# Kernel tuning notes

Hardware: AMD Instinct MI355X
Metric: run time of the kernel (lower is better)

The kernel has to match this reference:

```python
import jax, jax.numpy as jnp
import numpy as np

B, V, C, H, W, D, G = 1, 5, 32, 128, 160, 48, 1


def _bilinear_sample(fea, x, y):
    # fea: [B,C,H,W]; x,y: [B,N] pixel coords (grid_sample align_corners=True, zero padding)
    Bb, Cc, Hh, Ww = fea.shape
    x0 = jnp.floor(x); y0 = jnp.floor(y)
    x1 = x0 + 1.0; y1 = y0 + 1.0
    wx1 = x - x0; wx0 = 1.0 - wx1
    wy1 = y - y0; wy0 = 1.0 - wy1
    flat = fea.reshape(Bb, Cc, Hh * Ww)
    def gather(xi, yi):
        valid = (xi >= 0) & (xi <= Ww - 1) & (yi >= 0) & (yi <= Hh - 1)
        xc = jnp.clip(xi, 0, Ww - 1).astype(jnp.int32)
        yc = jnp.clip(yi, 0, Hh - 1).astype(jnp.int32)
        idx = (yc * Ww + xc)[:, None, :]                      # [B,1,N]
        g = jnp.take_along_axis(flat, idx, axis=2)            # [B,C,N]
        return g * valid[:, None, :].astype(fea.dtype)
    return (gather(x0, y0) * (wx0 * wy0)[:, None, :]
          + gather(x1, y0) * (wx1 * wy0)[:, None, :]
          + gather(x0, y1) * (wx0 * wy1)[:, None, :]
          + gather(x1, y1) * (wx1 * wy1)[:, None, :])          # [B,C,N]


def _homo_warp(src_fea, src_proj, ref_proj, depth_values):
    # src_fea [B,C,H,W]; src_proj/ref_proj [B,4,4]; depth_values [B,D,H,W]
    Bb, Cc, Hh, Ww = src_fea.shape
    Dd = depth_values.shape[1]
    proj = src_proj @ jnp.linalg.inv(ref_proj)
    rot, trans = proj[:, :3, :3], proj[:, :3, 3:4]
    yy, xx = jnp.meshgrid(jnp.arange(Hh, dtype=src_fea.dtype),
                          jnp.arange(Ww, dtype=src_fea.dtype), indexing='ij')
    xyz = jnp.stack([xx.ravel(), yy.ravel(), jnp.ones(Hh * Ww, src_fea.dtype)], 0)  # [3,HW]
    rot_xyz = jnp.einsum('bij,jn->bin', rot, xyz)                                    # [B,3,HW]
    d = depth_values.reshape(Bb, 1, Dd, Hh * Ww)
    pxyz = rot_xyz[:, :, None, :] * d + trans[:, :, :, None]                         # [B,3,D,HW]
    px = (pxyz[:, 0] / pxyz[:, 2]).reshape(Bb, -1)
    py = (pxyz[:, 1] / pxyz[:, 2]).reshape(Bb, -1)
    warped = _bilinear_sample(src_fea, px, py)                                       # [B,C,D*HW]
    return warped.reshape(Bb, Cc, Dd, Hh, Ww)


def _pixelwise_net(sim, w0, b0, w1, b1, w2, b2):
    # sim [B,G,D,H,W]; 1x1x1 convs; BatchNorm at default init in eval is identity
    x = jax.nn.relu(jnp.einsum('oc,bcdhw->bodhw', w0, sim) + b0[None, :, None, None, None])
    x = jax.nn.relu(jnp.einsum('oc,bcdhw->bodhw', w1, x) + b1[None, :, None, None, None])
    x = jnp.einsum('oc,bcdhw->bodhw', w2, x) + b2[None, :, None, None, None]
    p = jax.nn.sigmoid(x[:, 0])                       # [B,D,H,W]
    return jnp.max(p, axis=1, keepdims=True)          # [B,1,H,W]


def _fuse_proj(p):
    # p [B,2,4,4] -> extrinsics with K folded into top 3x4
    top = jnp.einsum('bij,bjk->bik', p[:, 1, :3, :3], p[:, 0, :3, :4])
    return p[:, 0].at[:, :3, :4].set(top)


def _forward(features, proj_matrices, depth_values, w0, b0, w1, b1, w2, b2, reg_w, reg_b, num_depth):
    ref_fea = features[0]
    Bb, Cc, Hh, Ww = ref_fea.shape
    ref_proj = _fuse_proj(proj_matrices[:, 0])
    ref_vol = ref_fea.reshape(Bb, G, Cc // G, 1, Hh, Ww)
    sim_sum = 0.0
    wsum = 1e-5
    vw_list = []
    for i in range(1, features.shape[0]):
        src_proj = _fuse_proj(proj_matrices[:, i])
        warped = _homo_warp(features[i], src_proj, ref_proj, depth_values)
        warped = warped.reshape(Bb, G, Cc // G, num_depth, Hh, Ww)
        sim = (warped * ref_vol).mean(2)              # [B,G,D,H,W]
        vw = _pixelwise_net(sim, w0, b0, w1, b1, w2, b2)   # [B,1,H,W]
        vw_list.append(vw)
        sim_sum = sim_sum + sim * vw[:, None]
        wsum = wsum + vw[:, None]
    sim = sim_sum / wsum
    cost = jax.lax.conv_general_dilated(sim, reg_w, (1, 1, 1), 'SAME',
                                        dimension_numbers=('NCDHW', 'OIDHW', 'NCDHW'))
    prob_volume_pre = cost[:, 0] + reg_b[0]           # [B,D,H,W]
    prob = jax.nn.softmax(prob_volume_pre, axis=1)
    idx = jnp.argmax(prob, axis=1, keepdims=True)
    depth = jnp.take_along_axis(depth_values, idx, axis=1)[:, 0]   # winner-take-all depth
    conf = jnp.max(prob, axis=1)
    view_weights = jnp.concatenate(vw_list, axis=1)
    return depth, conf, prob, view_weights


def setup_inputs() -> dict:
    key = jax.random.key(0)
    ks = jax.random.split(key, 6)
    features = jax.random.normal(ks[0], (V, B, C, H, W), jnp.float32)
    # Plausible camera geometry: identity-ish extrinsics + pinhole intrinsics
    K = np.eye(4, dtype=np.float32)
    K[0, 0] = K[1, 1] = 150.0; K[0, 2] = W / 2.0; K[1, 2] = H / 2.0
    mats = []
    for v in range(V):
        E = np.eye(4, dtype=np.float32)
        a = 0.01 * v
        ca, sa = np.cos(a), np.sin(a)
        E[:3, :3] = np.array([[ca, 0, sa], [0, 1, 0], [-sa, 0, ca]], np.float32)
        E[0, 3] = -5.0 * v
        mats.append(np.stack([E, K], 0))
    proj_matrices = jnp.asarray(np.stack(mats, 0)[None])  # [1,V,2,4,4]
    depth_values = jnp.broadcast_to(
        jnp.linspace(425.0, 935.0, D, dtype=jnp.float32).reshape(1, D, 1, 1), (B, D, H, W)) * jnp.ones((B, D, H, W), jnp.float32)
    return {
        'features': features,
        'proj_matrices': proj_matrices,
        'depth_values': depth_values,
        'w0': jax.random.normal(ks[1], (16, G), jnp.float32) * 0.1,
        'b0': jnp.zeros((16,), jnp.float32),
        'w1': jax.random.normal(ks[2], (8, 16), jnp.float32) * 0.1,
        'b1': jnp.zeros((8,), jnp.float32),
        'w2': jax.random.normal(ks[3], (1, 8), jnp.float32) * 0.1,
        'b2': jnp.zeros((1,), jnp.float32),
        'reg_w': jax.random.normal(ks[4], (1, G, 3, 3, 3), jnp.float32) * 0.1,
        'reg_b': jnp.zeros((1,), jnp.float32),
        'num_depth': D,
    }


def reference(features, proj_matrices, depth_values, w0, b0, w1, b1, w2, b2, reg_w, reg_b, num_depth):
    return _forward(features, proj_matrices, depth_values, w0, b0, w1, b1, w2, b2, reg_w, reg_b, num_depth)
```

## Files before the change

kernel.cpp:

```cpp
#include <hip/hip_runtime.h>
#include <hip/hip_bf16.h>
#include <math.h>

#define W_  160
#define H_  128
#define HW  20480
#define D_  48
#define C_  32
#define NV  4

#define TX  16
#define TY  4
#define TXH 18
#define TYH 6
#define NCOL (TXH*TYH)
#define GD  4
#define GDS 12

template<int CTRL>
__device__ __forceinline__ float dpp_add(float s) {
  int t = __builtin_amdgcn_update_dpp(0, __float_as_int(s), CTRL, 0xF, 0xF, true);
  return s + __int_as_float(t);
}

__device__ __forceinline__ unsigned ordf(float f) {
  unsigned b = __float_as_uint(f);
  return b ^ (((int)b >> 31) | 0x80000000u);
}
__device__ __forceinline__ float deordf(unsigned u) {
  unsigned b = (u & 0x80000000u) ? (u ^ 0x80000000u) : ~u;
  return __uint_as_float(b);
}

__device__ __forceinline__ void fuse_proj(const float* pm, float* P) {
  const float* E = pm;
  const float* K = pm + 16;
  for (int r = 0; r < 3; ++r)
    for (int c = 0; c < 4; ++c)
      P[r*4+c] = K[r*4+0]*E[0*4+c] + K[r*4+1]*E[1*4+c] + K[r*4+2]*E[2*4+c];
  for (int c = 0; c < 4; ++c) P[12+c] = E[12+c];
}

__device__ void invert4(const float* m, float* invOut) {
  float inv[16];
  inv[0]  =  m[5]*m[10]*m[15] - m[5]*m[11]*m[14] - m[9]*m[6]*m[15] + m[9]*m[7]*m[14] + m[13]*m[6]*m[11] - m[13]*m[7]*m[10];
  inv[4]  = -m[4]*m[10]*m[15] + m[4]*m[11]*m[14] + m[8]*m[6]*m[15] - m[8]*m[7]*m[14] - m[12]*m[6]*m[11] + m[12]*m[7]*m[10];
  inv[8]  =  m[4]*m[9]*m[15]  - m[4]*m[11]*m[13] - m[8]*m[5]*m[15] + m[8]*m[7]*m[13] + m[12]*m[5]*m[11] - m[12]*m[7]*m[9];
  inv[12] = -m[4]*m[9]*m[14]  + m[4]*m[10]*m[13] + m[8]*m[5]*m[14] - m[8]*m[6]*m[13] - m[12]*m[5]*m[10] + m[12]*m[6]*m[9];
  inv[1]  = -m[1]*m[10]*m[15] + m[1]*m[11]*m[14] + m[9]*m[2]*m[15] - m[9]*m[3]*m[14] - m[13]*m[2]*m[11] + m[13]*m[3]*m[10];
  inv[5]  =  m[0]*m[10]*m[15] - m[0]*m[11]*m[14] - m[8]*m[2]*m[15] + m[8]*m[3]*m[14] + m[12]*m[2]*m[11] - m[12]*m[3]*m[10];
  inv[9]  = -m[0]*m[9]*m[15]  + m[0]*m[11]*m[13] + m[8]*m[1]*m[15] - m[8]*m[3]*m[13] - m[12]*m[1]*m[11] + m[12]*m[3]*m[9];
  inv[13] =  m[0]*m[9]*m[14]  - m[0]*m[10]*m[13] - m[8]*m[1]*m[14] + m[8]*m[2]*m[13] + m[12]*m[1]*m[10] - m[12]*m[2]*m[9];
  inv[2]  =  m[1]*m[6]*m[15]  - m[1]*m[7]*m[14]  - m[5]*m[2]*m[15] + m[5]*m[3]*m[14] + m[13]*m[2]*m[7]  - m[13]*m[3]*m[6];
  inv[6]  = -m[0]*m[6]*m[15]  + m[0]*m[7]*m[14]  + m[4]*m[2]*m[15] - m[4]*m[3]*m[14] - m[12]*m[2]*m[7]  + m[12]*m[3]*m[6];
  inv[10] =  m[0]*m[5]*m[15]  - m[0]*m[7]*m[13]  - m[4]*m[1]*m[15] + m[4]*m[3]*m[13] + m[12]*m[1]*m[7]  - m[12]*m[3]*m[5];
  inv[14] = -m[0]*m[5]*m[14]  + m[0]*m[6]*m[13]  + m[4]*m[1]*m[14] - m[4]*m[2]*m[13] - m[12]*m[1]*m[6]  + m[12]*m[2]*m[5];
  inv[3]  = -m[1]*m[6]*m[11]  + m[1]*m[7]*m[10]  + m[5]*m[2]*m[11] - m[5]*m[3]*m[10] - m[9]*m[2]*m[7]   + m[9]*m[3]*m[6];
  inv[7]  =  m[0]*m[6]*m[11]  - m[0]*m[7]*m[10]  - m[4]*m[2]*m[11] + m[4]*m[3]*m[10] + m[8]*m[2]*m[7]   - m[8]*m[3]*m[6];
  inv[11] = -m[0]*m[5]*m[11]  + m[0]*m[7]*m[9]   + m[4]*m[1]*m[11] - m[4]*m[3]*m[9]  - m[8]*m[1]*m[7]   + m[8]*m[3]*m[5];
  inv[15] =  m[0]*m[5]*m[10]  - m[0]*m[6]*m[9]   - m[4]*m[1]*m[10] + m[4]*m[2]*m[9]  + m[8]*m[1]*m[6]   - m[8]*m[2]*m[5];
  float det = m[0]*inv[0] + m[1]*inv[4] + m[2]*inv[8] + m[3]*inv[12];
  det = 1.0f / det;
  for (int i = 0; i < 16; i++) invOut[i] = inv[i] * det;
}

__global__ void __launch_bounds__(256)
k_prep(const float* __restrict__ feat, const float* __restrict__ pm,
       float* __restrict__ tf, float* __restrict__ xf,
       unsigned* __restrict__ vwu) {
  __shared__ float tile[C_][64+1];
  int v  = blockIdx.y;
  int p0 = blockIdx.x * 64;
  int t  = threadIdx.x;

  if (v == 0) vwu[blockIdx.x*256 + t] = 0u;

  int pl = t & 63;
  int cg = t >> 6;
  const float* src = feat + (size_t)v*C_*HW + p0 + pl;
  #pragma unroll
  for (int k = 0; k < 8; ++k) {
    int c = cg*8 + k;
    tile[c][pl] = src[(size_t)c*HW];
  }
  __syncthreads();

  int pp = t >> 2;
  int co = (t & 3) * 8;
  float4 a, b;
  a.x = tile[co+0][pp]; a.y = tile[co+1][pp]; a.z = tile[co+2][pp]; a.w = tile[co+3][pp];
  b.x = tile[co+4][pp]; b.y = tile[co+5][pp]; b.z = tile[co+6][pp]; b.w = tile[co+7][pp];
  float* dst = tf + ((size_t)v*HW + p0 + pp)*C_ + co;
  *(float4*)dst = a;
  *(float4*)(dst+4) = b;

  if (blockIdx.x == 0 && v == 0) {
    if (t < 64) tf[(size_t)5*HW*C_ + t] = 0.0f;
    if (t == 0) {
      float Pr[16], Pinv[16], Ps[16], M[16];
      fuse_proj(pm, Pr);
      invert4(Pr, Pinv);
      for (int vv = 1; vv <= NV; ++vv) {
        fuse_proj(pm + vv*32, Ps);
        for (int r = 0; r < 4; ++r)
          for (int c = 0; c < 4; ++c) {
            float acc = 0.f;
            for (int k = 0; k < 4; ++k) acc += Ps[r*4+k]*Pinv[k*4+c];
            M[r*4+c] = acc;
          }
        float* o = xf + (vv-1)*12;
        o[0]=M[0];  o[1]=M[1];  o[2]=M[2];
        o[3]=M[4];  o[4]=M[5];  o[5]=M[6];
        o[6]=M[8];  o[7]=M[9];  o[8]=M[10];
        o[9]=M[3];  o[10]=M[7]; o[11]=M[11];
      }
    }
  }
}

template<int KX>
__device__ __forceinline__ void build_tab(
    const char* tfb, int chb, int ZB, float4 rfc,
    int xmin, int ymin, int ch, float* tabp) {
  #pragma unroll
  for (int t = 0; t < KX*3; ++t) {
    int xi = xmin + t/3;
    int yi = ymin + t%3;
    bool valid = ((unsigned)xi < (unsigned)W_) && ((unsigned)yi < (unsigned)H_);
    int off = valid ? (yi*W_ + xi)*(C_*4) : ZB;
    float4 a = *(const float4*)(tfb + off + chb);
    float d = a.x*rfc.x + a.y*rfc.y + a.z*rfc.z + a.w*rfc.w;
    d = dpp_add<0xB1>(d);
    d = dpp_add<0x4E>(d);
    d = dpp_add<0x141>(d);
    if (ch == (t & 7)) tabp[t] = d;
  }
}

__global__ void __launch_bounds__(256)
k_warp(const float* __restrict__ tf, const float* __restrict__ dv,
       const float* __restrict__ xf, float* __restrict__ sim4) {
  __shared__ float dtab[4][8][37];

  int lane = threadIdx.x & 63;
  int wv = threadIdx.x >> 6;
  int ch = lane & 7;
  int pix = (lane >> 3) & 7;
  int wvg = __builtin_amdgcn_readfirstlane((blockIdx.x*256 + threadIdx.x) >> 6);
  const int PGPV = HW/8;
  int pg = wvg % PGPV;
  int v  = wvg / PGPV;
  int p  = pg*8 + pix;

  float xpix = (float)(p % W_);
  float ypix = (float)(p / W_);

  const float* M = xf + v*12;
  float rx = M[0]*xpix + M[1]*ypix + M[2];
  float ry = M[3]*xpix + M[4]*ypix + M[5];
  float rz = M[6]*xpix + M[7]*ypix + M[8];
  float t0 = M[9], t1 = M[10], t2 = M[11];

  float4 rfc = *(const float4*)(tf + (size_t)p*C_ + ch*4);
  rfc.x *= (1.0f/(float)C_); rfc.y *= (1.0f/(float)C_);
  rfc.z *= (1.0f/(float)C_); rfc.w *= (1.0f/(float)C_);

  const char* tfb = (const char*)(tf + (size_t)(v+1)*HW*C_);
  const int chb = ch*16;
  const int ZB = (4-v)*HW*C_*4;

  float depE0 = dv[p];
  float depE1 = dv[(size_t)47*HW + p];
  float dpk[6];
  #pragma unroll
  for (int k = 0; k < 6; ++k) dpk[k] = dv[(size_t)(k*8 + ch)*HW + p];

  float Z0 = rz*depE0 + t2, Z1 = rz*depE1 + t2;
  float iz0 = 1.0f / Z0,     iz1 = 1.0f / Z1;
  float pxa = (rx*depE0 + t0) * iz0, pya = (ry*depE0 + t1) * iz0;
  float pxb = (rx*depE1 + t0) * iz1, pyb = (ry*depE1 + t1) * iz1;
  int xmin = (int)floorf(fminf(pxa, pxb));
  int ymin = (int)floorf(fminf(pya, pyb));
  int Nx = (int)floorf(fmaxf(pxa, pxb)) - xmin + 2;
  int Ny = (int)floorf(fmaxf(pya, pyb)) - ymin + 2;

  float dmn = fminf(depE0, depE1), dmx = fmaxf(depE0, depE1);
  bool ok = (Nx <= 12) && (Ny <= 3) && (Z0*Z1 > 0.0f);
  #pragma unroll
  for (int k = 0; k < 6; ++k) ok = ok && (dpk[k] >= dmn) && (dpk[k] <= dmx);

  float* simv = sim4 + (size_t)p*4 + v;

  if (__all(ok)) {
    float* tabp = dtab[wv][pix];
    int xhi;
    if (__all(Nx <= 5)) {
      build_tab<5>(tfb, chb, ZB, rfc, xmin, ymin, ch, tabp);
      xhi = xmin + 3;
    } else if (__all(Nx <= 8)) {
      build_tab<8>(tfb, chb, ZB, rfc, xmin, ymin, ch, tabp);
      xhi = xmin + 6;
    } else {
      build_tab<12>(tfb, chb, ZB, rfc, xmin, ymin, ch, tabp);
      xhi = xmin + 10;
    }

    #pragma unroll
    for (int k = 0; k < 6; ++k) {
      float dep = dpk[k];
      float Z  = rz*dep + t2;
      float zr = 1.0f / Z;
      float px = (rx*dep + t0) * zr;
      float py = (ry*dep + t1) * zr;
      int xi = (int)floorf(px);
      int yi = (int)floorf(py);
      xi = min(max(xi, xmin), xhi);
      yi = min(max(yi, ymin), ymin + 1);
      float wx1 = px - (float)xi;
      float wy1 = py - (float)yi;
      float wx0 = 1.0f - wx1, wy0 = 1.0f - wy1;
      int idx = (xi - xmin)*3 + (yi - ymin);
      float t00 = tabp[idx];
      float t01 = tabp[idx + 3];
      float t10 = tabp[idx + 1];
      float t11 = tabp[idx + 4];
      float s = wx0*wy0*t00 + wx1*wy0*t01 + wx0*wy1*t10 + wx1*wy1*t11;
      if (ch == ch) ;
      simv[(size_t)(k*8 + ch)*HW*4] = s;
    }
  } else {
    const float* tff  = tf + (size_t)(v+1)*HW*C_;
    const float* refp = tf + (size_t)p*C_;
    const int ZE = (4-v)*HW*C_;
    #pragma unroll 1
    for (int k = 0; k < 6; ++k) {
      float dep = dpk[k];
      float Z  = rz*dep + t2;
      float px = (rx*dep + t0) / Z;
      float py = (ry*dep + t1) / Z;
      float x0f = floorf(px), y0f = floorf(py);
      float wx1 = px - x0f, wy1 = py - y0f;
      float wx0 = 1.0f - wx1, wy0 = 1.0f - wy1;
      int x0 = (int)x0f, y0 = (int)y0f;
      int x1 = x0 + 1,   y1 = y0 + 1;
      bool vx0 = ((unsigned)x0 <= (unsigned)(W_-1));
      bool vx1 = ((unsigned)x1 <= (unsigned)(W_-1));
      bool vy0 = ((unsigned)y0 <= (unsigned)(H_-1));
      bool vy1 = ((unsigned)y1 <= (unsigned)(H_-1));
      int cx0 = min(max(x0, 0), W_-1);
      int cx1 = min(max(x1, 0), W_-1);
      int cy0 = min(max(y0, 0), H_-1);
      int cy1 = min(max(y1, 0), H_-1);
      int o00 = (vx0 && vy0) ? (cy0*W_+cx0)*C_ : ZE;
      int o01 = (vx1 && vy0) ? (cy0*W_+cx1)*C_ : ZE;
      int o10 = (vx0 && vy1) ? (cy1*W_+cx0)*C_ : ZE;
      int o11 = (vx1 && vy1) ? (cy1*W_+cx1)*C_ : ZE;
      float a00=0.f, a01=0.f, a10=0.f, a11=0.f;
      #pragma unroll 1
      for (int q = 0; q < 8; ++q) {
        float4 rq = *(const float4*)(refp + q*4);
        float4 c0 = *(const float4*)(tff + o00 + q*4);
        float4 c1 = *(const float4*)(tff + o01 + q*4);
        float4 c2 = *(const float4*)(tff + o10 + q*4);
        float4 c3 = *(const float4*)(tff + o11 + q*4);
        a00 += c0.x*rq.x + c0.y*rq.y + c0.z*rq.z + c0.w*rq.w;
        a01 += c1.x*rq.x + c1.y*rq.y + c1.z*rq.z + c1.w*rq.w;
        a10 += c2.x*rq.x + c2.y*rq.y + c2.z*rq.z + c2.w*rq.w;
        a11 += c3.x*rq.x + c3.y*rq.y + c3.z*rq.z + c3.w*rq.w;
      }
      float s = (wx0*wy0*a00 + wx1*wy0*a01 + wx0*wy1*a10 + wx1*wy1*a11)
                * (1.0f/(float)C_);
      simv[(size_t)(k*8 + ch)*HW*4] = s;
    }
  }
}

__global__ void __launch_bounds__(256)
k_mlp(const float* __restrict__ sim4,
      const float* __restrict__ w0, const float* __restrict__ b0,
      const float* __restrict__ w1, const float* __restrict__ b1,
      const float* __restrict__ w2, const float* __restrict__ b2,
      unsigned* __restrict__ vwu) {
  int idx = blockIdx.x*blockDim.x + threadIdx.x;
  if (idx >= D_*HW) return;
  int p = idx % HW;

  float4 s4 = *(const float4*)(sim4 + (size_t)idx*4);

  float y0, y1, y2, y3;
  {
    float acc[4][8];
    #pragma unroll
    for (int j = 0; j < 8; ++j) {
      float bb = b1[j];
      acc[0][j] = bb; acc[1][j] = bb; acc[2][j] = bb; acc[3][j] = bb;
    }
    #pragma unroll
    for (int o = 0; o < 16; ++o) {
      float wo = w0[o], bo = b0[o];
      float h0 = fmaxf(fmaf(wo, s4.x, bo), 0.0f);
      float h1 = fmaxf(fmaf(wo, s4.y, bo), 0.0f);
      float h2 = fmaxf(fmaf(wo, s4.z, bo), 0.0f);
      float h3 = fmaxf(fmaf(wo, s4.w, bo), 0.0f);
      #pragma unroll
      for (int j = 0; j < 8; ++j) {
        float w = w1[j*16+o];
        acc[0][j] = fmaf(w, h0, acc[0][j]);
        acc[1][j] = fmaf(w, h1, acc[1][j]);
        acc[2][j] = fmaf(w, h2, acc[2][j]);
        acc[3][j] = fmaf(w, h3, acc[3][j]);
      }
    }
    float b2v = b2[0];
    y0 = b2v; y1 = b2v; y2 = b2v; y3 = b2v;
    #pragma unroll
    for (int j = 0; j < 8; ++j) {
      float w = w2[j];
      y0 = fmaf(w, fmaxf(acc[0][j], 0.0f), y0);
      y1 = fmaf(w, fmaxf(acc[1][j], 0.0f), y1);
      y2 = fmaf(w, fmaxf(acc[2][j], 0.0f), y2);
      y3 = fmaf(w, fmaxf(acc[3][j], 0.0f), y3);
    }
  }
  atomicMax(&vwu[0*HW + p], ordf(y0));
  atomicMax(&vwu[1*HW + p], ordf(y1));
  atomicMax(&vwu[2*HW + p], ordf(y2));
  atomicMax(&vwu[3*HW + p], ordf(y3));
}

__global__ void __launch_bounds__(256)
k_fusecv(const float* __restrict__ sim4, const unsigned* __restrict__ vwu,
         const float* __restrict__ rw, const float* __restrict__ rb,
         float* __restrict__ cost) {
  __shared__ float svw[NV][NCOL];
  __shared__ float sinvw[NCOL];
  __shared__ int   sgpc[NCOL];
  __shared__ float sfus[GDS+2][TYH][TXH+1];

  int tid = threadIdx.x;
  int gx0 = blockIdx.x*TX;
  int gy0 = blockIdx.y*TY;
  int g   = blockIdx.z;

  if (tid < NCOL) {
    int yy = tid / TXH, xx = tid % TXH;
    int gy = gy0 + yy - 1, gx = gx0 + xx - 1;
    bool valid = (gx >= 0) && (gx < W_) && (gy >= 0) && (gy < H_);
    int gp = min(max(gy,0),H_-1)*W_ + min(max(gx,0),W_-1);
    sgpc[tid] = gp;
    float a0 = 1.0f/(1.0f + expf(-deordf(vwu[0*HW+gp])));
    float a1 = 1.0f/(1.0f + expf(-deordf(vwu[1*HW+gp])));
    float a2 = 1.0f/(1.0f + expf(-deordf(vwu[2*HW+gp])));
    float a3 = 1.0f/(1.0f + expf(-deordf(vwu[3*HW+gp])));
    float inv = valid ? 1.0f/(1e-5f + a0+a1+a2+a3) : 0.0f;
    if (!valid) { a0=a1=a2=a3=0.f; }
    svw[0][tid]=a0; svw[1][tid]=a1; svw[2][tid]=a2; svw[3][tid]=a3;
    sinvw[tid] = inv;
  }
  __syncthreads();

  for (int j = tid; j < (GDS+2)*NCOL; j += 256) {
    int s = j / NCOL, r = j % NCOL;
    int dz = g*GDS - 1 + s;
    float val = 0.0f;
    if (dz >= 0 && dz < D_) {
      int gp = sgpc[r];
      float4 s4 = *(const float4*)(sim4 + ((size_t)dz*HW + gp)*4);
      val = (s4.x*svw[0][r] + s4.y*svw[1][r] + s4.z*svw[2][r] + s4.w*svw[3][r])
            * sinvw[r];
    }
    sfus[s][r/TXH][r%TXH] = val;
  }
  __syncthreads();

  {
    int pid = tid & 63;
    int dg  = tid >> 6;
    int px = pid & 15, py = pid >> 4;
    float kw[27];
    #pragma unroll
    for (int i = 0; i < 27; ++i) kw[i] = rw[i];
    float bias = rb[0];
    int gp = (gy0+py)*W_ + gx0+px;

    #pragma unroll
    for (int k = 0; k < 3; ++k) {
      int dl = dg*3 + k;
      float acc = bias;
      #pragma unroll
      for (int kd = 0; kd < 3; ++kd)
        #pragma unroll
        for (int ky = 0; ky < 3; ++ky)
          #pragma unroll
          for (int kx = 0; kx < 3; ++kx)
            acc += sfus[dl+kd][py+ky][px+kx] * kw[(kd*3+ky)*3+kx];
      cost[(size_t)(g*GDS + dl)*HW + gp] = acc;
    }
  }
}

__global__ void __launch_bounds__(256)
k_softmax(const float* __restrict__ cost, const unsigned* __restrict__ vwu,
          const float* __restrict__ dv, float* __restrict__ out) {
  int p = blockIdx.x*256 + threadIdx.x;
  if (p >= HW) return;

  float c[D_];
  #pragma unroll
  for (int d = 0; d < D_; ++d) c[d] = cost[(size_t)d*HW + p];

  float vmax = c[0];
  int am = 0;
  #pragma unroll
  for (int d = 1; d < D_; ++d) {
    if (c[d] > vmax) { vmax = c[d]; am = d; }
  }
  float sum = 0.0f;
  #pragma unroll
  for (int d = 0; d < D_; ++d) {
    float e = expf(c[d] - vmax);
    c[d] = e;
    sum += e;
  }
  float inv = 1.0f / sum;
  #pragma unroll
  for (int d = 0; d < D_; ++d)
    out[(size_t)(2*HW) + (size_t)d*HW + p] = c[d] * inv;

  out[p] = dv[(size_t)am*HW + p];
  out[HW + p] = inv;
  #pragma unroll
  for (int v = 0; v < NV; ++v)
    out[(size_t)(2*HW + D_*HW) + (size_t)v*HW + p] =
        1.0f/(1.0f + expf(-deordf(vwu[(size_t)v*HW + p])));
}

extern "C" void kernel_launch(void* const* d_in, const int* in_sizes, int n_in,
                              void* d_out, int out_size, void* d_ws, size_t ws_size,
                              hipStream_t stream) {
  const float* feat = (const float*)d_in[0];
  const float* pm   = (const float*)d_in[1];
  const float* dv   = (const float*)d_in[2];
  const float* w0   = (const float*)d_in[3];
  const float* b0   = (const float*)d_in[4];
  const float* w1   = (const float*)d_in[5];
  const float* b1   = (const float*)d_in[6];
  const float* w2   = (const float*)d_in[7];
  const float* b2   = (const float*)d_in[8];
  const float* rw   = (const float*)d_in[9];
  const float* rb   = (const float*)d_in[10];
  float* out = (float*)d_out;
  float* ws  = (float*)d_ws;

  float*    xf   = ws;
  float*    tf   = ws + 64;
  float*    sim4 = ws + 3276928;
  unsigned* vwu  = (unsigned*)(ws + 7209088);
  float*    cost = ws + 7291008;

  hipLaunchKernelGGL(k_prep, dim3(HW/64, 5), dim3(256), 0, stream,
                     feat, pm, tf, xf, vwu);
  hipLaunchKernelGGL(k_warp, dim3((NV*HW*8)/256), dim3(256), 0, stream,
                     tf, dv, xf, sim4);
  hipLaunchKernelGGL(k_mlp, dim3((D_*HW)/256), dim3(256), 0, stream,
                     sim4, w0, b0, w1, b1, w2, b2, vwu);
  hipLaunchKernelGGL(k_fusecv, dim3(W_/TX, H_/TY, GD), dim3(256), 0, stream,
                     sim4, vwu, rw, rb, cost);
  hipLaunchKernelGGL(k_softmax, dim3(HW/256), dim3(256), 0, stream,
                     cost, vwu, dv, out);
}
```

Before: 75.86 us.

## Fuse MLP, cost-volume fusion and softmax into one cooperative kernel

Merges the last three kernels into a single cooperative persistent kernel, with grid-wide syncs in place of kernel boundaries and grid-stride loops over work. The aim is to remove two launch gaps and their tail drain. In exchange it assumes 256 CUs when sizing the grid, limits parallelism to the resident block count, and pays for grid.sync barriers. The old three-kernel path stays as a fallback.

Result: slower. 212.6 us (+180.2%).

```diff
diff --git a/kernel.cpp b/kernel.cpp
--- a/kernel.cpp
+++ b/kernel.cpp
@@ -1,6 +1,9 @@
 #include <hip/hip_runtime.h>
 #include <hip/hip_bf16.h>
+#include <hip/hip_cooperative_groups.h>
 #include <math.h>
+
+namespace cg = cooperative_groups;
 
 #define W_  160
 #define H_  128
@@ -16,6 +19,7 @@
 #define NCOL (TXH*TYH)
 #define GD  4
 #define GDS 12
+#define NTILE (10*32*GD)
 
 template<int CTRL>
 __device__ __forceinline__ float dpp_add(float s) {
@@ -76,11 +80,11 @@
   if (v == 0) vwu[blockIdx.x*256 + t] = 0u;
 
   int pl = t & 63;
-  int cg = t >> 6;
+  int cg_ = t >> 6;
   const float* src = feat + (size_t)v*C_*HW + p0 + pl;
   #pragma unroll
   for (int k = 0; k < 8; ++k) {
-    int c = cg*8 + k;
+    int c = cg_*8 + k;
     tile[c][pl] = src[(size_t)c*HW];
   }
   __syncthreads();
@@ -225,7 +229,6 @@
       float t10 = tabp[idx + 1];
       float t11 = tabp[idx + 4];
       float s = wx0*wy0*t00 + wx1*wy0*t01 + wx0*wy1*t10 + wx1*wy1*t11;
-      if (ch == ch) ;
       simv[(size_t)(k*8 + ch)*HW*4] = s;
     }
   } else {
@@ -275,73 +278,52 @@
   }
 }
 
-__global__ void __launch_bounds__(256)
-k_mlp(const float* __restrict__ sim4,
-      const float* __restrict__ w0, const float* __restrict__ b0,
-      const float* __restrict__ w1, const float* __restrict__ b1,
-      const float* __restrict__ w2, const float* __restrict__ b2,
-      unsigned* __restrict__ vwu) {
-  int idx = blockIdx.x*blockDim.x + threadIdx.x;
-  if (idx >= D_*HW) return;
-  int p = idx % HW;
-
-  float4 s4 = *(const float4*)(sim4 + (size_t)idx*4);
-
-  float y0, y1, y2, y3;
-  {
-    float acc[4][8];
+__device__ __forceinline__ void mlp4(float4 s4,
+    const float* __restrict__ w0, const float* __restrict__ b0,
+    const float* __restrict__ w1, const float* __restrict__ b1,
+    const float* __restrict__ w2, const float* __restrict__ b2,
+    float& y0, float& y1, float& y2, float& y3) {
+  float acc[4][8];
+  #pragma unroll
+  for (int j = 0; j < 8; ++j) {
+    float bb = b1[j];
+    acc[0][j] = bb; acc[1][j] = bb; acc[2][j] = bb; acc[3][j] = bb;
+  }
+  #pragma unroll
+  for (int o = 0; o < 16; ++o) {
+    float wo = w0[o], bo = b0[o];
+    float h0 = fmaxf(fmaf(wo, s4.x, bo), 0.0f);
+    float h1 = fmaxf(fmaf(wo, s4.y, bo), 0.0f);
+    float h2 = fmaxf(fmaf(wo, s4.z, bo), 0.0f);
+    float h3 = fmaxf(fmaf(wo, s4.w, bo), 0.0f);
     #pragma unroll
     for (int j = 0; j < 8; ++j) {
-      float bb = b1[j];
-      acc[0][j] = bb; acc[1][j] = bb; acc[2][j] = bb; acc[3][j] = bb;
-    }
-    #pragma unroll
-    for (int o = 0; o < 16; ++o) {
-      float wo = w0[o], bo = b0[o];
-      float h0 = fmaxf(fmaf(wo, s4.x, bo), 0.0f);
-      float h1 = fmaxf(fmaf(wo, s4.y, bo), 0.0f);
-      float h2 = fmaxf(fmaf(wo, s4.z, bo), 0.0f);
-      float h3 = fmaxf(fmaf(wo, s4.w, bo), 0.0f);
-      #pragma unroll
-      for (int j = 0; j < 8; ++j) {
-        float w = w1[j*16+o];
-        acc[0][j] = fmaf(w, h0, acc[0][j]);
-        acc[1][j] = fmaf(w, h1, acc[1][j]);
-        acc[2][j] = fmaf(w, h2, acc[2][j]);
-        acc[3][j] = fmaf(w, h3, acc[3][j]);
-      }
-    }
-    float b2v = b2[0];
-    y0 = b2v; y1 = b2v; y2 = b2v; y3 = b2v;
-    #pragma unroll
-    for (int j = 0; j < 8; ++j) {
-      float w = w2[j];
-      y0 = fmaf(w, fmaxf(acc[0][j], 0.0f), y0);
-      y1 = fmaf(w, fmaxf(acc[1][j], 0.0f), y1);
-      y2 = fmaf(w, fmaxf(acc[2][j], 0.0f), y2);
-      y3 = fmaf(w, fmaxf(acc[3][j], 0.0f), y3);
-    }
-  }
-  atomicMax(&vwu[0*HW + p], ordf(y0));
-  atomicMax(&vwu[1*HW + p], ordf(y1));
-  atomicMax(&vwu[2*HW + p], ordf(y2));
-  atomicMax(&vwu[3*HW + p], ordf(y3));
-}
-
-__global__ void __launch_bounds__(256)
-k_fusecv(const float* __restrict__ sim4, const unsigned* __restrict__ vwu,
-         const float* __restrict__ rw, const float* __restrict__ rb,
-         float* __restrict__ cost) {
-  __shared__ float svw[NV][NCOL];
-  __shared__ float sinvw[NCOL];
-  __shared__ int   sgpc[NCOL];
-  __shared__ float sfus[GDS+2][TYH][TXH+1];
-
-  int tid = threadIdx.x;
-  int gx0 = blockIdx.x*TX;
-  int gy0 = blockIdx.y*TY;
-  int g   = blockIdx.z;
-
+      float w = w1[j*16+o];
+      acc[0][j] = fmaf(w, h0, acc[0][j]);
+      acc[1][j] = fmaf(w, h1, acc[1][j]);
+      acc[2][j] = fmaf(w, h2, acc[2][j]);
+      acc[3][j] = fmaf(w, h3, acc[3][j]);
+    }
+  }
+  float b2v = b2[0];
+  y0 = b2v; y1 = b2v; y2 = b2v; y3 = b2v;
+  #pragma unroll
+  for (int j = 0; j < 8; ++j) {
+    float w = w2[j];
+    y0 = fmaf(w, fmaxf(acc[0][j], 0.0f), y0);
+    y1 = fmaf(w, fmaxf(acc[1][j], 0.0f), y1);
+    y2 = fmaf(w, fmaxf(acc[2][j], 0.0f), y2);
+    y3 = fmaf(w, fmaxf(acc[3][j], 0.0f), y3);
+  }
+}
+
+__device__ __forceinline__ void fusecv_tile(
+    int g, int gx0, int gy0, int tid,
+    const float* __restrict__ sim4, const unsigned* __restrict__ vwu,
+    const float* __restrict__ rw, const float* __restrict__ rb,
+    float* __restrict__ cost,
+    float (*svw)[NCOL], float* sinvw, int* sgpc,
+    float (*sfus)[TYH][TXH+1]) {
   if (tid < NCOL) {
     int yy = tid / TXH, xx = tid % TXH;
     int gy = gy0 + yy - 1, gx = gx0 + xx - 1;
@@ -399,40 +381,125 @@
   }
 }
 
+__device__ __forceinline__ void softmax_px(
+    int p, const float* __restrict__ cost, const unsigned* __restrict__ vwu,
+    const float* __restrict__ dv, float* __restrict__ out) {
+  float c[D_];
+  #pragma unroll
+  for (int d = 0; d < D_; ++d) c[d] = cost[(size_t)d*HW + p];
+
+  float vmax = c[0];
+  int am = 0;
+  #pragma unroll
+  for (int d = 1; d < D_; ++d) {
+    if (c[d] > vmax) { vmax = c[d]; am = d; }
+  }
+  float sum = 0.0f;
+  #pragma unroll
+  for (int d = 0; d < D_; ++d) {
+    float e = expf(c[d] - vmax);
+    c[d] = e;
+    sum += e;
+  }
+  float inv = 1.0f / sum;
+  #pragma unroll
+  for (int d = 0; d < D_; ++d)
+    out[(size_t)(2*HW) + (size_t)d*HW + p] = c[d] * inv;
+
+  out[p] = dv[(size_t)am*HW + p];
+  out[HW + p] = inv;
+  #pragma unroll
+  for (int v = 0; v < NV; ++v)
+    out[(size_t)(2*HW + D_*HW) + (size_t)v*HW + p] =
+        1.0f/(1.0f + expf(-deordf(vwu[(size_t)v*HW + p])));
+}
+
+__global__ void __launch_bounds__(256)
+k_tail(const float* __restrict__ sim4,
+       const float* __restrict__ w0, const float* __restrict__ b0,
+       const float* __restrict__ w1, const float* __restrict__ b1,
+       const float* __restrict__ w2, const float* __restrict__ b2,
+       unsigned* __restrict__ vwu,
+       const float* __restrict__ rw, const float* __restrict__ rb,
+       const float* __restrict__ dv,
+       float* __restrict__ cost, float* __restrict__ out, int nb) {
+  cg::grid_group gg = cg::this_grid();
+
+  __shared__ float svw[NV][NCOL];
+  __shared__ float sinvw[NCOL];
+  __shared__ int   sgpc[NCOL];
+  __shared__ float sfus[GDS+2][TYH][TXH+1];
+
+  int bid = blockIdx.x;
+  int tid = threadIdx.x;
+
+  for (int idx = bid*256 + tid; idx < D_*HW; idx += nb*256) {
+    int p = idx % HW;
+    float4 s4 = *(const float4*)(sim4 + (size_t)idx*4);
+    float y0, y1, y2, y3;
+    mlp4(s4, w0, b0, w1, b1, w2, b2, y0, y1, y2, y3);
+    atomicMax(&vwu[0*HW + p], ordf(y0));
+    atomicMax(&vwu[1*HW + p], ordf(y1));
+    atomicMax(&vwu[2*HW + p], ordf(y2));
+    atomicMax(&vwu[3*HW + p], ordf(y3));
+  }
+
+  gg.sync();
+
+  for (int t = bid; t < NTILE; t += nb) {
+    __syncthreads();
+    int g   = t / 320;
+    int rem = t % 320;
+    int gy0 = (rem / 10) * TY;
+    int gx0 = (rem % 10) * TX;
+    fusecv_tile(g, gx0, gy0, tid, sim4, vwu, rw, rb, cost,
+                svw, sinvw, sgpc, sfus);
+  }
+
+  gg.sync();
+
+  for (int p = bid*256 + tid; p < HW; p += nb*256)
+    softmax_px(p, cost, vwu, dv, out);
+}
+
+__global__ void __launch_bounds__(256)
+k_mlp(const float* __restrict__ sim4,
+      const float* __restrict__ w0, const float* __restrict__ b0,
+      const float* __restrict__ w1, const float* __restrict__ b1,
+      const float* __restrict__ w2, const float* __restrict__ b2,
+      unsigned* __restrict__ vwu) {
+  int idx = blockIdx.x*blockDim.x + threadIdx.x;
+  if (idx >= D_*HW) return;
+  int p = idx % HW;
+  float4 s4 = *(const float4*)(sim4 + (size_t)idx*4);
+  float y0, y1, y2, y3;
+  mlp4(s4, w0, b0, w1, b1, w2, b2, y0, y1, y2, y3);
+  atomicMax(&vwu[0*HW + p], ordf(y0));
+  atomicMax(&vwu[1*HW + p], ordf(y1));
+  atomicMax(&vwu[2*HW + p], ordf(y2));
+  atomicMax(&vwu[3*HW + p], ordf(y3));
+}
+
+__global__ void __launch_bounds__(256)
+k_fusecv(const float* __restrict__ sim4, const unsigned* __restrict__ vwu,
+         const float* __restrict__ rw, const float* __restrict__ rb,
+         float* __restrict__ cost) {
+  __shared__ float svw[NV][NCOL];
+  __shared__ float sinvw[NCOL];
+  __shared__ int   sgpc[NCOL];
+  __shared__ float sfus[GDS+2][TYH][TXH+1];
+  int gx0 = blockIdx.x*TX;
+  int gy0 = blockIdx.y*TY;
+  fusecv_tile(blockIdx.z, gx0, gy0, threadIdx.x, sim4, vwu, rw, rb, cost,
+              svw, sinvw, sgpc, sfus);
+}
+
 __global__ void __launch_bounds__(256)
 k_softmax(const float* __restrict__ cost, const unsigned* __restrict__ vwu,
           const float* __restrict__ dv, float* __restrict__ out) {
   int p = blockIdx.x*256 + threadIdx.x;
   if (p >= HW) return;
-
-  float c[D_];
-  #pragma unroll
-  for (int d = 0; d < D_; ++d) c[d] = cost[(size_t)d*HW + p];
-
-  float vmax = c[0];
-  int am = 0;
-  #pragma unroll
-  for (int d = 1; d < D_; ++d) {
-    if (c[d] > vmax) { vmax = c[d]; am = d; }
-  }
-  float sum = 0.0f;
-  #pragma unroll
-  for (int d = 0; d < D_; ++d) {
-    float e = expf(c[d] - vmax);
-    c[d] = e;
-    sum += e;
-  }
-  float inv = 1.0f / sum;
-  #pragma unroll
-  for (int d = 0; d < D_; ++d)
-    out[(size_t)(2*HW) + (size_t)d*HW + p] = c[d] * inv;
-
-  out[p] = dv[(size_t)am*HW + p];
-  out[HW + p] = inv;
-  #pragma unroll
-  for (int v = 0; v < NV; ++v)
-    out[(size_t)(2*HW + D_*HW) + (size_t)v*HW + p] =
-        1.0f/(1.0f + expf(-deordf(vwu[(size_t)v*HW + p])));
+  softmax_px(p, cost, vwu, dv, out);
 }
 
 extern "C" void kernel_launch(void* const* d_in, const int* in_sizes, int n_in,
@@ -462,6 +529,21 @@
                      feat, pm, tf, xf, vwu);
   hipLaunchKernelGGL(k_warp, dim3((NV*HW*8)/256), dim3(256), 0, stream,
                      tf, dv, xf, sim4);
+
+  int maxPerCU = 0;
+  hipError_t qe = hipOccupancyMaxActiveBlocksPerMultiprocessor(
+      &maxPerCU, (const void*)k_tail, 256, 0);
+  int nb = (qe == hipSuccess) ? maxPerCU * 256 : 0;
+  if (nb > 2048) nb = 2048;
+
+  if (nb >= 256) {
+    void* args[] = { (void*)&sim4, (void*)&w0, (void*)&b0, (void*)&w1, (void*)&b1,
+                     (void*)&w2, (void*)&b2, (void*)&vwu, (void*)&rw, (void*)&rb,
+                     (void*)&dv, (void*)&cost, (void*)&out, (void*)&nb };
+    hipError_t le = hipLaunchCooperativeKernel((void*)k_tail, dim3(nb), dim3(256),
+                                               args, 0, stream);
+    if (le == hipSuccess) return;
+  }
   hipLaunchKernelGGL(k_mlp, dim3((D_*HW)/256), dim3(256), 0, stream,
                      sim4, w0, b0, w1, b1, w2, b2, vwu);
   hipLaunchKernelGGL(k_fusecv, dim3(W_/TX, H_/TY, GD), dim3(256), 0, stream,
```
